# Kernel tuning notes

Measured on AMD Instinct MI355X. Metric: run time of the kernel, lower is better.

## Reference

```python
import jax, jax.numpy as jnp
import numpy as np

B, T, S, H, E = 4, 2048, 2048, 16, 64  # batch, q_len, kv_len, heads, head_dim


def setup_inputs() -> dict:
    key = jax.random.key(0)
    kq, kk, kv, kl, kw = jax.random.split(key, 5)
    query = jax.random.normal(kq, (B, T, H * E), dtype=jnp.float32)
    key_t = jax.random.normal(kk, (B, S, H * E), dtype=jnp.float32)
    value = jax.random.normal(kv, (B, S, H * E), dtype=jnp.float32)
    # valid lengths in [S//2, S] so every row has at least one attendable key
    lengths = jax.random.randint(kl, (B,), S // 2, S + 1)
    key_padding_mask = jnp.arange(S)[None, :] < lengths[:, None]  # (B, S) bool, True = keep
    W_out = jax.random.normal(kw, (H * E, E), dtype=jnp.float32) * 0.02
    b_out = jnp.zeros((E,), dtype=jnp.float32)
    return {"query": query, "key": key_t, "value": value,
            "key_padding_mask": key_padding_mask, "W_out": W_out, "b_out": b_out}


def reference(query, key, value, key_padding_mask, W_out, b_out):
    # (B, N, H*E) -> (B, H, N, E)
    q = query.reshape(B, T, H, E).transpose(0, 2, 1, 3)
    k = key.reshape(B, S, H, E).transpose(0, 2, 1, 3)
    v = value.reshape(B, S, H, E).transpose(0, 2, 1, 3)
    softmax_temp = 1.0 / np.sqrt(E).astype(np.float32)
    scores = jnp.einsum('bhte,bhse->bhts', q * softmax_temp, k)  # (B,H,T,S)
    neg_inf = jnp.finfo(scores.dtype).min
    scores = jnp.where(key_padding_mask[:, None, None, :], scores, neg_inf)
    attn = jax.nn.softmax(scores, axis=-1)  # dropout p=0 -> identity
    out = jnp.einsum('bhts,bhsd->bthd', attn, v)  # (B,T,H,E)
    out = out.reshape(B * T, H * E)
    return out @ W_out + b_out  # (B*T, E)
```

## Files before the change

### kernel.cpp

```cpp
#include <hip/hip_runtime.h>
#include <hip/hip_bf16.h>

#define Bq 4
#define Tq 2048
#define Sq 2048
#define Hq 16
#define Eq 64
#define HEq 1024

typedef __attribute__((ext_vector_type(8))) _Float16 half8;
typedef __attribute__((ext_vector_type(16))) float f32x16;

#define AS1 __attribute__((address_space(1)))
#define AS3 __attribute__((address_space(3)))

__device__ __forceinline__ void gl_lds16(const void* g, void* l) {
  __builtin_amdgcn_global_load_lds((const AS1 unsigned*)g, (AS3 unsigned*)l, 16, 0, 0);
}
#define VMCNT(n) asm volatile("s_waitcnt vmcnt(" #n ")" ::: "memory")
#define LGKM0 asm volatile("s_waitcnt lgkmcnt(0)" ::: "memory")

#if __has_builtin(__builtin_amdgcn_exp2f)
#define EXP2F(x) __builtin_amdgcn_exp2f(x)
#else
#define EXP2F(x) exp2f(x)
#endif

__device__ __forceinline__ unsigned pk16(float a, float b) {
  return __builtin_bit_cast(unsigned, __builtin_amdgcn_cvt_pkrtz(a, b));
}

__global__ __launch_bounds__(256) void prep_kernel(
    const float* __restrict__ K, const float* __restrict__ V,
    const float* __restrict__ W, const void* __restrict__ mask,
    char* __restrict__ KP, char* __restrict__ VP,
    _Float16* __restrict__ WT, int* __restrict__ lens) {
  __shared__ _Float16 tile[64][72];
  const int bid = blockIdx.x;
  const int tid = threadIdx.x;

  if (bid < 4096) {
    const int isV = bid >= 2048;
    const int b2 = bid & 2047;
    const int t = b2 & 31, h = (b2 >> 5) & 15, b = b2 >> 9;
    const int s0 = t * 64;
    const int s_in = tid >> 2, e0 = (tid & 3) * 16;
    const float* X = isV ? V : K;
    const float* src = X + ((size_t)(b * Sq + s0 + s_in) * HEq + h * Eq + e0);
#pragma unroll
    for (int i = 0; i < 4; ++i) {
      const float4 f = *(const float4*)(src + i * 4);
      tile[s_in][e0 + i * 4 + 0] = (_Float16)f.x;
      tile[s_in][e0 + i * 4 + 1] = (_Float16)f.y;
      tile[s_in][e0 + i * 4 + 2] = (_Float16)f.z;
      tile[s_in][e0 + i * 4 + 3] = (_Float16)f.w;
    }
    __syncthreads();
    half8 u0, u1;
    if (!isV) {
      const int gi = tid >> 5, sl = (tid & 31) * 2;
#pragma unroll
      for (int j = 0; j < 8; ++j) {
        u0[j] = tile[sl][gi * 8 + j];
        u1[j] = tile[sl + 1][gi * 8 + j];
      }
      char* dst = KP + ((size_t)b2 * 8192) + tid * 32;
      *(half8*)dst = u0;
      *(half8*)(dst + 16) = u1;
    } else {
      const int g = tid >> 5, e = (tid & 31) * 2;
#pragma unroll
      for (int j = 0; j < 8; ++j) {
        const int row = ((g >> 2) << 5) + (((g >> 1) & 1) << 4) +
                        ((j >> 2) << 3) + ((g & 1) << 2) +
                        (((j >> 1) & 1) << 1) + (j & 1);
        u0[j] = tile[row][e];
        u1[j] = tile[row][e + 1];
      }
      char* dst = VP + ((size_t)b2 * 8192) + tid * 32;
      *(half8*)dst = u0;
      *(half8*)(dst + 16) = u1;
    }
  } else if (bid < 4352) {
    const int id = (bid - 4096) * 256 + tid;
    const int n = id >> 10, k = id & 1023;
    WT[id] = (_Float16)W[k * Eq + n];
  } else if (tid < 64) {
    const int b = bid - 4352;
    const int lane = tid;
    const unsigned w0 = *(const unsigned*)mask;
    int cnt = 0;
    if (w0 == 1u) {
      const int* m = (const int*)mask + b * Sq;
      for (int s = lane; s < Sq; s += 64) cnt += (m[s] != 0);
    } else if (w0 == 0x3F800000u) {
      const float* m = (const float*)mask + b * Sq;
      for (int s = lane; s < Sq; s += 64) cnt += (m[s] != 0.f);
    } else {
      const unsigned char* m = (const unsigned char*)mask + b * Sq;
      for (int s = lane; s < Sq; s += 64) cnt += (m[s] != 0);
    }
    for (int o = 32; o; o >>= 1) cnt += __shfl_down(cnt, o);
    if (lane == 0) lens[b] = cnt;
  }
}

__global__ __launch_bounds__(512, 4) void flash_kernel(
    const float* __restrict__ Q, const char* __restrict__ KP,
    const char* __restrict__ VP, const int* __restrict__ lens,
    _Float16* __restrict__ attnO) {
  __shared__ __align__(16) _Float16 KV[4][2][4096];

  const int bid = blockIdx.x;
  const int qt = bid >> 6;
  const int h = (bid >> 2) & 15;
  const int b = ((bid & 3) + (bid >> 8)) & 3;
  const int tid = threadIdx.x;
  const int w = tid >> 6, lane = tid & 63;
  const int qq = lane & 31, hi = lane >> 5;
  const int len = lens[b];
  const int q0 = qt * 256 + w * 32;

  const float qscale = 0.125f * 1.44269504088896340736f;
  half8 qf[4];
  {
    const float* qrow = Q + ((size_t)(b * Tq + q0 + qq) * HEq + h * Eq);
#pragma unroll
    for (int kw = 0; kw < 4; ++kw) {
      const float4 f0 = *(const float4*)(qrow + kw * 16 + hi * 8);
      const float4 f1 = *(const float4*)(qrow + kw * 16 + hi * 8 + 4);
      half8 qv;
      qv[0] = (_Float16)(f0.x * qscale);
      qv[1] = (_Float16)(f0.y * qscale);
      qv[2] = (_Float16)(f0.z * qscale);
      qv[3] = (_Float16)(f0.w * qscale);
      qv[4] = (_Float16)(f1.x * qscale);
      qv[5] = (_Float16)(f1.y * qscale);
      qv[6] = (_Float16)(f1.z * qscale);
      qv[7] = (_Float16)(f1.w * qscale);
      qf[kw] = qv;
    }
  }

  f32x16 Oa[2];
#pragma unroll
  for (int i = 0; i < 2; ++i)
#pragma unroll
    for (int r = 0; r < 16; ++r) Oa[i][r] = 0.f;
  float ls0 = 0.f, ls1 = 0.f;

  const char* kpb = KP + (size_t)(b * Hq + h) * 32 * 8192;
  const char* vpb = VP + (size_t)(b * Hq + h) * 32 * 8192;
  const int so = w * 1024 + lane * 16;

  const int nt = (len + 63) >> 6;

  gl_lds16(kpb + so, (char*)&KV[0][0][0] + so);
  gl_lds16(vpb + so, (char*)&KV[0][1][0] + so);
  gl_lds16(kpb + 8192 + so, (char*)&KV[1][0][0] + so);
  gl_lds16(vpb + 8192 + so, (char*)&KV[1][1][0] + so);

  for (int t = 0; t < nt; ++t) {
    {
      const int tp = (t + 2 < nt) ? t + 2 : nt - 1;
      const size_t tb = (size_t)tp * 8192;
      gl_lds16(kpb + tb + so, (char*)&KV[(t + 2) & 3][0][0] + so);
      gl_lds16(vpb + tb + so, (char*)&KV[(t + 2) & 3][1][0] + so);
    }
    VMCNT(4);
    __builtin_amdgcn_s_barrier();
    __builtin_amdgcn_sched_barrier(0);

    const char* kbuf = (const char*)&KV[t & 3][0][0];
    const char* vbuf = (const char*)&KV[t & 3][1][0];

    __builtin_amdgcn_s_setprio(1);
    f32x16 sc[2];
#pragma unroll
    for (int sm = 0; sm < 2; ++sm) {
      f32x16 acc;
#pragma unroll
      for (int r = 0; r < 16; ++r) acc[r] = 0.f;
#pragma unroll
      for (int kw = 0; kw < 4; ++kw) {
        const half8 kf = *(const half8*)(kbuf + (kw * 2 + hi) * 1024 +
                                         (sm * 32 + qq) * 16);
        acc = __builtin_amdgcn_mfma_f32_32x32x16_f16(kf, qf[kw], acc, 0, 0, 0);
      }
      sc[sm] = acc;
    }
    __builtin_amdgcn_s_setprio(0);

    const int svalid = len - (t << 6);
    if (svalid < 64) {
#pragma unroll
      for (int r = 0; r < 16; ++r) {
        const int sl = (r & 3) + 8 * (r >> 2) + 4 * hi;
        if (sl >= svalid) sc[0][r] = -60000.f;
        if (32 + sl >= svalid) sc[1][r] = -60000.f;
      }
    }

    unsigned pku[2][4][2];
#pragma unroll
    for (int sm = 0; sm < 2; ++sm)
#pragma unroll
      for (int rb = 0; rb < 4; ++rb)
#pragma unroll
        for (int pp = 0; pp < 2; ++pp) {
          const float a0 = EXP2F(sc[sm][rb * 4 + pp * 2]);
          const float a1 = EXP2F(sc[sm][rb * 4 + pp * 2 + 1]);
          ls0 += a0;
          ls1 += a1;
          pku[sm][rb][pp] = pk16(a0, a1);
        }

#pragma unroll
    for (int kw = 0; kw < 4; ++kw) {
      const int sm = kw >> 1;
      const int rbe = (kw & 1) * 2, rbo = rbe + 1;
      union { unsigned u[4]; half8 h; } pu;
      pu.u[0] = pku[sm][rbe][0];
      pu.u[1] = pku[sm][rbe][1];
      pu.u[2] = pku[sm][rbo][0];
      pu.u[3] = pku[sm][rbo][1];
      const half8 pf = pu.h;
      __builtin_amdgcn_s_setprio(1);
#pragma unroll
      for (int eh = 0; eh < 2; ++eh) {
        const half8 vf = *(const half8*)(vbuf + (kw * 2 + hi) * 1024 +
                                         (eh * 32 + qq) * 16);
        Oa[eh] = __builtin_amdgcn_mfma_f32_32x32x16_f16(vf, pf, Oa[eh], 0, 0, 0);
      }
      __builtin_amdgcn_s_setprio(0);
    }
  }

  VMCNT(0);
  __builtin_amdgcn_s_barrier();
  __builtin_amdgcn_sched_barrier(0);

  float ls = ls0 + ls1;
  ls += __shfl_xor(ls, 32);
  const float inv = 1.f / ls;
  char* const scratch = (char*)&KV[0][0][0] + w * 4096;
#pragma unroll
  for (int eh = 0; eh < 2; ++eh)
#pragma unroll
    for (int rb = 0; rb < 4; ++rb)
#pragma unroll
      for (int pp2 = 0; pp2 < 2; ++pp2) {
        const int e0 = eh * 32 + rb * 8 + hi * 4 + pp2 * 2;
        const unsigned uo = pk16(Oa[eh][rb * 4 + pp2 * 2] * inv,
                                 Oa[eh][rb * 4 + pp2 * 2 + 1] * inv);
        *(unsigned*)(scratch + qq * 128 + ((e0 * 2) ^ ((qq & 7) << 4))) = uo;
      }
  LGKM0;
  __builtin_amdgcn_sched_barrier(0);
#pragma unroll
  for (int i = 0; i < 4; ++i) {
    const int qr = i * 8 + (lane >> 3), ch = lane & 7;
    const half8 ov = *(const half8*)(scratch + qr * 128 + ((ch * 16) ^ ((qr & 7) << 4)));
    *(half8*)(attnO + (size_t)(b * Tq + q0 + qr) * HEq + h * Eq + ch * 8) = ov;
  }
}

typedef __attribute__((ext_vector_type(4))) float floatx4;
__global__ __launch_bounds__(128) void proj_kernel(
    const _Float16* __restrict__ A, const _Float16* __restrict__ WT,
    const float* __restrict__ bias, float* __restrict__ out) {
  const int tid = threadIdx.x;
  const int w = tid >> 6, lane = tid & 63;
  const int g = lane >> 4, c = lane & 15;
  const int r0 = blockIdx.x * 32 + w * 16;
  floatx4 acc[4];
#pragma unroll
  for (int i = 0; i < 4; ++i) acc[i] = (floatx4){0.f, 0.f, 0.f, 0.f};
  const _Float16* arow = A + (size_t)(r0 + c) * HEq;
  for (int kc = 0; kc < 32; ++kc) {
    const half8 af = *(const half8*)(arow + kc * 32 + g * 8);
#pragma unroll
    for (int nt = 0; nt < 4; ++nt) {
      const half8 bf =
          *(const half8*)(WT + (size_t)(nt * 16 + c) * HEq + kc * 32 + g * 8);
      acc[nt] = __builtin_amdgcn_mfma_f32_16x16x32_f16(af, bf, acc[nt], 0, 0, 0);
    }
  }
#pragma unroll
  for (int r = 0; r < 4; ++r) {
    const int row = r0 + g * 4 + r;
#pragma unroll
    for (int nt = 0; nt < 4; ++nt) {
      const int col = nt * 16 + c;
      out[(size_t)row * Eq + col] = acc[nt][r] + bias[col];
    }
  }
}

extern "C" void kernel_launch(void* const* d_in, const int* in_sizes, int n_in,
                              void* d_out, int out_size, void* d_ws, size_t ws_size,
                              hipStream_t stream) {
  const float* q = (const float*)d_in[0];
  const float* k = (const float*)d_in[1];
  const float* v = (const float*)d_in[2];
  const void* mask = d_in[3];
  const float* W = (const float*)d_in[4];
  const float* bias = (const float*)d_in[5];
  float* out = (float*)d_out;

  char* ws = (char*)d_ws;
  int* lens = (int*)ws;
  _Float16* WT = (_Float16*)(ws + 256);
  _Float16* attn = (_Float16*)(ws + (256 + 131072));
  char* KP = ws + (256 + 131072 + (1 << 24));
  char* VP = ws + (256 + 131072 + 2 * (1 << 24));

  prep_kernel<<<4356, 256, 0, stream>>>(k, v, W, mask, KP, VP, WT, lens);
  flash_kernel<<<512, 512, 0, stream>>>(q, KP, VP, lens, attn);
  proj_kernel<<<256, 128, 0, stream>>>(attn, WT, bias, out);
}
```

Measured before the change: 94.59 us.

## Load K/V fragments directly from global memory instead of staging through LDS

Removes the four-buffer global-to-LDS async prefetch pipeline, along with its waitcnt and barrier synchronisation and the setprio hints. Each wave now reads its K and V MFMA operands straight from global memory using the same packed layout. LDS is cut to a 32 KB scratch used only for the output transpose, which allows more resident blocks and removes the per-tile barriers. In exchange, all eight waves fetch the same K/V tiles redundantly through the caches, and there is no explicit prefetch to hide global load latency.

```diff
diff --git a/kernel.cpp b/kernel.cpp
--- a/kernel.cpp
+++ b/kernel.cpp
@@ -11,13 +11,6 @@
 typedef __attribute__((ext_vector_type(8))) _Float16 half8;
 typedef __attribute__((ext_vector_type(16))) float f32x16;
 
-#define AS1 __attribute__((address_space(1)))
-#define AS3 __attribute__((address_space(3)))
-
-__device__ __forceinline__ void gl_lds16(const void* g, void* l) {
-  __builtin_amdgcn_global_load_lds((const AS1 unsigned*)g, (AS3 unsigned*)l, 16, 0, 0);
-}
-#define VMCNT(n) asm volatile("s_waitcnt vmcnt(" #n ")" ::: "memory")
 #define LGKM0 asm volatile("s_waitcnt lgkmcnt(0)" ::: "memory")
 
 #if __has_builtin(__builtin_amdgcn_exp2f)
@@ -109,7 +102,7 @@
     const float* __restrict__ Q, const char* __restrict__ KP,
     const char* __restrict__ VP, const int* __restrict__ lens,
     _Float16* __restrict__ attnO) {
-  __shared__ __align__(16) _Float16 KV[4][2][4096];
+  __shared__ __align__(16) char scratch_lds[8][4096];
 
   const int bid = blockIdx.x;
   const int qt = bid >> 6;
@@ -151,30 +144,13 @@
 
   const char* kpb = KP + (size_t)(b * Hq + h) * 32 * 8192;
   const char* vpb = VP + (size_t)(b * Hq + h) * 32 * 8192;
-  const int so = w * 1024 + lane * 16;
-
+  const int koff = hi * 1024 + qq * 16;
   const int nt = (len + 63) >> 6;
 
-  gl_lds16(kpb + so, (char*)&KV[0][0][0] + so);
-  gl_lds16(vpb + so, (char*)&KV[0][1][0] + so);
-  gl_lds16(kpb + 8192 + so, (char*)&KV[1][0][0] + so);
-  gl_lds16(vpb + 8192 + so, (char*)&KV[1][1][0] + so);
-
   for (int t = 0; t < nt; ++t) {
-    {
-      const int tp = (t + 2 < nt) ? t + 2 : nt - 1;
-      const size_t tb = (size_t)tp * 8192;
-      gl_lds16(kpb + tb + so, (char*)&KV[(t + 2) & 3][0][0] + so);
-      gl_lds16(vpb + tb + so, (char*)&KV[(t + 2) & 3][1][0] + so);
-    }
-    VMCNT(4);
-    __builtin_amdgcn_s_barrier();
-    __builtin_amdgcn_sched_barrier(0);
-
-    const char* kbuf = (const char*)&KV[t & 3][0][0];
-    const char* vbuf = (const char*)&KV[t & 3][1][0];
-
-    __builtin_amdgcn_s_setprio(1);
+    const char* kbuf = kpb + (size_t)t * 8192;
+    const char* vbuf = vpb + (size_t)t * 8192;
+
     f32x16 sc[2];
 #pragma unroll
     for (int sm = 0; sm < 2; ++sm) {
@@ -183,13 +159,12 @@
       for (int r = 0; r < 16; ++r) acc[r] = 0.f;
 #pragma unroll
       for (int kw = 0; kw < 4; ++kw) {
-        const half8 kf = *(const half8*)(kbuf + (kw * 2 + hi) * 1024 +
-                                         (sm * 32 + qq) * 16);
+        const half8 kf =
+            *(const half8*)(kbuf + kw * 2048 + sm * 512 + koff);
         acc = __builtin_amdgcn_mfma_f32_32x32x16_f16(kf, qf[kw], acc, 0, 0, 0);
       }
       sc[sm] = acc;
     }
-    __builtin_amdgcn_s_setprio(0);
 
     const int svalid = len - (t << 6);
     if (svalid < 64) {
@@ -225,25 +200,19 @@
       pu.u[2] = pku[sm][rbo][0];
       pu.u[3] = pku[sm][rbo][1];
       const half8 pf = pu.h;
-      __builtin_amdgcn_s_setprio(1);
 #pragma unroll
       for (int eh = 0; eh < 2; ++eh) {
-        const half8 vf = *(const half8*)(vbuf + (kw * 2 + hi) * 1024 +
-                                         (eh * 32 + qq) * 16);
+        const half8 vf =
+            *(const half8*)(vbuf + kw * 2048 + hi * 1024 + (eh * 32 + qq) * 16);
         Oa[eh] = __builtin_amdgcn_mfma_f32_32x32x16_f16(vf, pf, Oa[eh], 0, 0, 0);
       }
-      __builtin_amdgcn_s_setprio(0);
-    }
-  }
-
-  VMCNT(0);
-  __builtin_amdgcn_s_barrier();
-  __builtin_amdgcn_sched_barrier(0);
+    }
+  }
 
   float ls = ls0 + ls1;
   ls += __shfl_xor(ls, 32);
   const float inv = 1.f / ls;
-  char* const scratch = (char*)&KV[0][0][0] + w * 4096;
+  char* const scratch = &scratch_lds[w][0];
 #pragma unroll
   for (int eh = 0; eh < 2; ++eh)
 #pragma unroll
```

After: 141.9 us. +50.0%, slower.
